# Optimization experiments

Hardware: AMD Instinct MI355X
Metric: run time of the kernel (lower is better)

## Reference

```python
import jax, jax.numpy as jnp
import numpy as np

B, S, D = 4, 2048, 1024


def setup_inputs() -> dict:
    key = jax.random.key(0)
    ks = jax.random.split(key, 9)
    scale = 1.0 / np.sqrt(D)
    x = jax.random.normal(ks[0], (B, S, D), dtype=jnp.float32)
    # causal mask (batch, seq, seq), int32; positions with 0 are masked out
    mask = jnp.broadcast_to(jnp.tril(jnp.ones((S, S), dtype=jnp.int32)), (B, S, S))
    Wq = jax.random.uniform(ks[1], (D, D), jnp.float32, -scale, scale)
    bq = jax.random.uniform(ks[2], (D,), jnp.float32, -scale, scale)
    Wk = jax.random.uniform(ks[3], (D, D), jnp.float32, -scale, scale)
    bk = jax.random.uniform(ks[4], (D,), jnp.float32, -scale, scale)
    Wv = jax.random.uniform(ks[5], (D, D), jnp.float32, -scale, scale)
    bv = jax.random.uniform(ks[6], (D,), jnp.float32, -scale, scale)
    Wo = jax.random.uniform(ks[7], (D, D), jnp.float32, -scale, scale)
    bo = jax.random.uniform(ks[8], (D,), jnp.float32, -scale, scale)
    return {"x": x, "mask": mask, "Wq": Wq, "bq": bq, "Wk": Wk, "bk": bk,
            "Wv": Wv, "bv": bv, "Wo": Wo, "bo": bo}


def reference(x, mask, Wq, bq, Wk, bk, Wv, bv, Wo, bo):
    d_model = x.shape[-1]
    scaling = jnp.sqrt(jnp.asarray(d_model, dtype=jnp.float32))
    # torch nn.Linear: y = x @ W.T + b
    Q = jnp.einsum('bsd,ed->bse', x, Wq) + bq
    K = jnp.einsum('bsd,ed->bse', x, Wk) + bk
    V = jnp.einsum('bsd,ed->bse', x, Wv) + bv
    scores = jnp.einsum('bqd,bkd->bqk', Q, K) / scaling  # (B, S, S)
    scores = jnp.where(mask == 0, jnp.float32(-1e9), scores)
    attn = jax.nn.softmax(scores, axis=2)
    out = jnp.einsum('bqk,bkd->bqd', attn, V)
    out = jnp.einsum('bsd,ed->bse', out, Wo) + bo
    return out, attn
```

## Files before the change

### kernel.cpp

```cpp
#include <hip/hip_runtime.h>
#include <hip/hip_bf16.h>
#include <stdint.h>


typedef unsigned short u16;
typedef __attribute__((ext_vector_type(8))) __bf16 bf16x8;
typedef __attribute__((ext_vector_type(4))) float f32x4;

__device__ __forceinline__ u16 f2bf(float f) {
  unsigned int u = __builtin_bit_cast(unsigned int, f);
  u = u + 0x7FFFu + ((u >> 16) & 1u);
  return (u16)(u >> 16);
}

__device__ __forceinline__ float bf2f(u16 u) {
  unsigned int w = ((unsigned int)u) << 16;
  return __builtin_bit_cast(float, w);
}

__device__ __forceinline__ void gl_lds16(const void* g, void* l) {
  __builtin_amdgcn_global_load_lds(
      (const __attribute__((address_space(1))) void*)g,
      (__attribute__((address_space(3))) void*)l, 16, 0, 0);
}

#define MFMA(a, b, c) __builtin_amdgcn_mfma_f32_16x16x32_bf16((a), (b), (c), 0, 0, 0)

#define TILE 128
#define BKK  64
template<int GM, int GX, int OUTMODE, bool BIAS, bool CKB, int NTT>
__global__ __launch_bounds__(256) void gemm_bt(
    const u16* __restrict__ A, const u16* __restrict__ Bmat,
    const float* __restrict__ b0, const float* __restrict__ b1,
    const float* __restrict__ b2,
    void* __restrict__ C0, u16* __restrict__ C1, u16* __restrict__ C2,
    int N, int K, long long sAb, long long sBb, long long sCb, int nchunk) {
  __shared__ __align__(16) u16 As[2][TILE * BKK];
  __shared__ __align__(16) u16 Bs[2][TILE * BKK];
  const int bid = blockIdx.x;
  int bx, by, bz;
  if (GM == 1) {
    const int lidx = (bid & 7) * nchunk + (bid >> 3);
    bz = lidx / 136;
    const int i = lidx - bz * 136;
    by = (int)((sqrtf(8.f * i + 1.f) - 1.f) * 0.5f);
    while ((by + 1) * (by + 2) / 2 <= i) ++by;
    while (by * (by + 1) / 2 > i) --by;
    bx = i - by * (by + 1) / 2;
  } else if (GM == 3) {
    const int j = bid & 255;
    const int k = j >> 5;
    by = (bid >> 8) ? k : 15 - k;
    bz = (j & 31) >> 3;
    bx = j & 7;
  } else if (GM == 4) {
    const int xcd = bid & 7, c = bid >> 3;
    bz = 0;
    by = xcd * 8 + (c >> 3);
    bx = c & 7;
  } else {
    const int lidx = (bid & 7) * 64 + (bid >> 3);
    bz = lidx >> 7;
    by = (lidx & 127) >> 4;
    bx = lidx & 15;
  }
  const int t = threadIdx.x;
  const int lane = t & 63, wid = t >> 6;
  const int wm = (wid >> 1) * 64, wn = (wid & 1) * 64;
  const int fr = lane & 15, fh = lane >> 4;

  const char* Ab = (const char*)(A + (size_t)bz * sAb + (size_t)by * TILE * K);
  const size_t rowstride = (size_t)K * 2;
  const size_t BOFF = (size_t)8 * TILE * rowstride;
  const char* Btile = (const char*)(Bmat + (size_t)bz * sBb + (size_t)bx * TILE * K);

  int srow[4], scol[4], slin[4];
#pragma unroll
  for (int c = 0; c < 4; ++c) {
    slin[c] = c * 4096 + t * 16;
    srow[c] = slin[c] >> 7;
    scol[c] = (slin[c] & 127) ^ ((srow[c] & 7) << 4);
  }

  int Keff = K;
  if (CKB) { int kb2 = (by + 1) * TILE; Keff = kb2 < K ? kb2 : K; }
  const int nkt = Keff / BKK;

#define STAGE(ko_, buf_, Bp_)                                                 \
  {                                                                           \
    _Pragma("unroll") for (int c = 0; c < 4; ++c) {                           \
      gl_lds16(Ab + (size_t)srow[c] * rowstride + (ko_) + scol[c],            \
               (char*)As[buf_] + slin[c]);                                    \
      gl_lds16((Bp_) + (size_t)srow[c] * rowstride + (ko_) + scol[c],         \
               (char*)Bs[buf_] + slin[c]);                                    \
    }                                                                         \
  }

  STAGE(0, 0, Btile)
  __syncthreads();

  int cur = 0;
  for (int tt = 0; tt < NTT; ++tt) {
    f32x4 acc[4][4];
#pragma unroll
    for (int m = 0; m < 4; ++m)
#pragma unroll
      for (int n = 0; n < 4; ++n) acc[m][n] = {0.f, 0.f, 0.f, 0.f};

    for (int kt = 0; kt < nkt; ++kt) {
      const bool last = (kt + 1 == nkt);
      if (!last) {
        STAGE((size_t)(kt + 1) * (BKK * 2), cur ^ 1, Btile)
      } else if (NTT > 1 && tt + 1 < NTT) {
        STAGE(0, cur ^ 1, Btile + BOFF)
      }
      const char* Ac = (const char*)As[cur];
      const char* Bc = (const char*)Bs[cur];
#pragma unroll
      for (int kk = 0; kk < BKK; kk += 32) {
        bf16x8 af[4], bg[4];
#pragma unroll
        for (int m = 0; m < 4; ++m) {
          int r = wm + m * 16 + fr;
          int cb = (kk * 2 + fh * 16) ^ ((r & 7) << 4);
          af[m] = *(const bf16x8*)(Ac + r * 128 + cb);
        }
#pragma unroll
        for (int n = 0; n < 4; ++n) {
          int r = wn + n * 16 + fr;
          int cb = (kk * 2 + fh * 16) ^ ((r & 7) << 4);
          bg[n] = *(const bf16x8*)(Bc + r * 128 + cb);
        }
#pragma unroll
        for (int m = 0; m < 4; ++m)
#pragma unroll
          for (int n = 0; n < 4; ++n)
            acc[m][n] = MFMA(af[m], bg[n], acc[m][n]);
      }
      if (!last) __syncthreads();
      cur ^= 1;
    }

    const int bxe = bx + 8 * tt;
    const int gm0 = by * TILE + wm, gn0 = bxe * TILE + wn;
#pragma unroll
    for (int n = 0; n < 4; ++n) {
      const int gc = gn0 + n * 16 + fr;
      float bvv = 0.f;
      if (BIAS) {
        if (OUTMODE == 3) {
          const int w = bxe >> 3;
          bvv = (w == 0 ? b0 : w == 1 ? b1 : b2)[gc & 1023];
        } else {
          bvv = b0[gc];
        }
      }
#pragma unroll
      for (int m = 0; m < 4; ++m) {
        const int gr0 = gm0 + m * 16 + fh * 4;
        float v[4];
#pragma unroll
        for (int j = 0; j < 4; ++j) v[j] = acc[m][n][j] + bvv;
        if (OUTMODE == 1) {
          float* C = (float*)C0 + (size_t)bz * sCb;
#pragma unroll
          for (int j = 0; j < 4; ++j) C[(size_t)(gr0 + j) * N + gc] = v[j];
        } else if (OUTMODE == 0) {
          u16* C = (u16*)C0 + (size_t)bz * sCb;
#pragma unroll
          for (int j = 0; j < 4; ++j) C[(size_t)(gr0 + j) * N + gc] = f2bf(v[j]);
        } else {
          const int w = bxe >> 3;
          const int gcl = gc & 1023;
          u16* dst = (w == 0) ? (u16*)C0 : (w == 1) ? C1 : C2;
          const float sc = (w == 0) ? 0.03125f : 1.0f;
#pragma unroll
          for (int j = 0; j < 4; ++j)
            dst[(size_t)(gr0 + j) * 1024 + gcl] = f2bf(v[j] * sc);
        }
      }
    }

    if (NTT > 1 && tt + 1 < NTT) {
      __syncthreads();
      Btile += BOFF;
    }
  }
#undef STAGE
}

#define WGFENCE asm volatile("" ::: "memory")
#define WGBAR()                         \
  {                                     \
    WGFENCE;                            \
    __builtin_amdgcn_s_barrier();       \
    WGFENCE;                            \
  }
#define LGKM0                                              \
  {                                                        \
    asm volatile("s_waitcnt lgkmcnt(0)" ::: "memory");     \
    __builtin_amdgcn_sched_barrier(0);                     \
  }
#define VMC(n_) asm volatile("s_waitcnt vmcnt(" #n_ ")" ::: "memory")

#define STG(dst_, srcb_, kt_, kh_)                                            \
  {                                                                           \
    _Pragma("unroll") for (int c_ = 0; c_ < 2; ++c_)                          \
        gl_lds16((srcb_) + (size_t)(c_ * 128 + srow0) * 2048 +                \
                     (kt_) * 128 + (kh_) * 64 + scol16,                       \
                 (char*)(dst_) + c_ * 8192 + t * 16);                         \
  }
#define LDA(slot_, mh_)                                                       \
  {                                                                           \
    _Pragma("unroll") for (int m_ = 0; m_ < 4; ++m_) {                        \
      const int r_ = WR + (mh_) * 64 + m_ * 16 + fr;                          \
      af[m_] = *(const bf16x8*)((const char*)(slot_) + r_ * 64 + fb);         \
    }                                                                         \
  }
#define LDB(slot_)                                                            \
  {                                                                           \
    _Pragma("unroll") for (int n_ = 0; n_ < 4; ++n_) {                        \
      const int r_ = WC + n_ * 16 + fr;                                       \
      bg[n_] = *(const bf16x8*)((const char*)(slot_) + r_ * 64 + fb);         \
    }                                                                         \
  }
#define MMAP(mh_)                                                             \
  {                                                                           \
    _Pragma("unroll") for (int m_ = 0; m_ < 4; ++m_)                          \
        _Pragma("unroll") for (int n_ = 0; n_ < 4; ++n_)                      \
            acc[(mh_) * 4 + m_][n_] =                                         \
                MFMA(af[m_], bg[n_], acc[(mh_) * 4 + m_][n_]);                \
  }
#define PHASE(CUR, KH, MH, DOB, VMSTMT, ...)   \
  {                                            \
    if (DOB) LDB(Bs[CUR][KH]);                 \
    LDA(As[CUR][KH], MH);                      \
    __VA_ARGS__;                               \
    WGBAR();                                   \
    LGKM0;                                     \
    __builtin_amdgcn_s_setprio(1);             \
    MMAP(MH);                                  \
    __builtin_amdgcn_s_setprio(0);             \
    VMSTMT;                                    \
    WGBAR();                                   \
  }

template <int LAUNCH>
__global__ __launch_bounds__(512, 2) void gemm256(
    const u16* __restrict__ xb, const u16* __restrict__ wqkb,
    const u16* __restrict__ wvb, const u16* __restrict__ wob,
    u16* __restrict__ qb, u16* __restrict__ kb, u16* __restrict__ vr,
    u16* __restrict__ pb, u16* __restrict__ vtb,
    const float* __restrict__ bq, const float* __restrict__ bk,
    const float* __restrict__ bv) {
  __shared__ __align__(16) u16 As[2][2][8192];
  __shared__ __align__(16) u16 Bs[2][2][8192];

  const int bid = blockIdx.x;
  const u16* Au;
  const u16* Bu;
  u16* Cu;
  const float* bias = nullptr;
  float scale = 1.f;
  int ldc, crow, ccol;
  if (LAUNCH == 0) {
    const int lidx = (bid & 7) * 32 + (bid >> 3);
    const int by = lidx >> 3, bx = lidx & 7;
    Au = xb + (size_t)by * 256 * 1024;
    Bu = wqkb + (size_t)bx * 256 * 1024;
    const int w = bx >> 2;
    Cu = w ? kb : qb;
    ldc = 1024;
    crow = by * 256;
    ccol = (bx & 3) * 256;
    bias = w ? bk : bq;
    scale = w ? 1.f : 0.03125f;
  } else if (LAUNCH == 1) {
    if (bid < 128) {
      const int by = bid >> 2, bx = bid & 3;
      Au = xb + (size_t)by * 256 * 1024;
      Bu = wvb + (size_t)bx * 256 * 1024;
      Cu = vr;
      ldc = 1024;
      crow = by * 256;
      ccol = bx * 256;
      bias = bv;
    } else {
      const int s2 = bid - 128;
      const int bz = s2 / 28;
      const int i = s2 - bz * 28;
      int by = 1, a2 = 0;
      while (a2 + by <= i) { a2 += by; ++by; }
      const int bx = i - a2;
      Au = qb + ((size_t)bz * 2048 + by * 256) * 1024;
      Bu = kb + ((size_t)bz * 2048 + bx * 256) * 1024;
      Cu = pb + (size_t)bz * 2048 * 2048;
      ldc = 2048;
      crow = by * 256;
      ccol = bx * 256;
    }
  } else {
    if (bid < 32) {
      const int bz = bid >> 3, d = bid & 7;
      Au = qb + ((size_t)bz * 2048 + d * 256) * 1024;
      Bu = kb + ((size_t)bz * 2048 + d * 256) * 1024;
      Cu = pb + (size_t)bz * 2048 * 2048;
      ldc = 2048;
      crow = d * 256;
      ccol = d * 256;
    } else {
      const int s2 = bid - 32;
      const int bz = s2 >> 5, j = s2 & 31;
      const int dby = j >> 3, sbx = j & 7;
      Au = wob + (size_t)dby * 256 * 1024;
      Bu = vr + ((size_t)bz * 2048 + sbx * 256) * 1024;
      Cu = vtb + (size_t)bz * 1024 * 2048;
      ldc = 2048;
      crow = dby * 256;
      ccol = sbx * 256;
    }
  }

  const int t = threadIdx.x;
  const int lane = t & 63, wid = t >> 6;
  const int WR = (wid >> 2) * 128, WC = (wid & 3) * 64;
  const int fr = lane & 15, fh = lane >> 4;
  const int fb = (fh ^ ((fr >> 1) & 3)) << 4;
  const int srow0 = t >> 2;
  const int scol16 = ((t & 3) ^ ((t >> 3) & 3)) << 4;
  const char* Abase = (const char*)Au;
  const char* Bbase = (const char*)Bu;

  f32x4 acc[8][4];
#pragma unroll
  for (int mi = 0; mi < 8; ++mi)
#pragma unroll
    for (int n = 0; n < 4; ++n) acc[mi][n] = {0.f, 0.f, 0.f, 0.f};
  bf16x8 af[4], bg[4];

  STG(As[0][0], Abase, 0, 0)
  STG(Bs[0][0], Bbase, 0, 0)
  STG(Bs[0][1], Bbase, 0, 1)
  STG(As[0][1], Abase, 0, 1)
  STG(Bs[1][0], Bbase, 1, 0)
  STG(As[1][0], Abase, 1, 0)
  STG(Bs[1][1], Bbase, 1, 1)
  VMC(10);
  WGBAR();

  for (int kt = 0; kt < 14; ++kt) {
    const int cur = kt & 1;
    PHASE(cur, 0, 0, true, (void)0, STG(As[cur ^ 1][1], Abase, kt + 1, 1))
    PHASE(cur, 0, 1, false, VMC(10), STG(Bs[cur][0], Bbase, kt + 2, 0))
    PHASE(cur, 1, 0, true, (void)0, STG(As[cur][0], Abase, kt + 2, 0))
    PHASE(cur, 1, 1, false, VMC(10), STG(Bs[cur][1], Bbase, kt + 2, 1))
  }
  PHASE(0, 0, 0, true, (void)0, STG(As[1][1], Abase, 15, 1))
  PHASE(0, 0, 1, false, VMC(8), (void)0)
  PHASE(0, 1, 0, true, (void)0, (void)0)
  PHASE(0, 1, 1, false, VMC(4), (void)0)
  PHASE(1, 0, 0, true, (void)0, (void)0)
  PHASE(1, 0, 1, false, VMC(0), (void)0)
  PHASE(1, 1, 0, true, (void)0, (void)0)
  PHASE(1, 1, 1, false, (void)0, (void)0)

  const int gr0 = crow + WR, gc0 = ccol + WC;
#pragma unroll
  for (int n = 0; n < 4; ++n) {
    const int gc = gc0 + n * 16 + fr;
    const float bb = bias ? bias[gc] : 0.f;
#pragma unroll
    for (int mi = 0; mi < 8; ++mi) {
      const int grr = gr0 + mi * 16 + fh * 4;
#pragma unroll
      for (int j = 0; j < 4; ++j)
        Cu[(size_t)(grr + j) * ldc + gc] = f2bf((acc[mi][n][j] + bb) * scale);
    }
  }
}

__global__ __launch_bounds__(256) void cvt_all(
    const float4* __restrict__ x, ushort4* __restrict__ xb,
    const float4* __restrict__ w0, const float4* __restrict__ w1,
    const float4* __restrict__ w2, const float4* __restrict__ w3,
    ushort4* __restrict__ o0, ushort4* __restrict__ o1,
    ushort4* __restrict__ o2, ushort4* __restrict__ o3) {
  int i = blockIdx.x * 256 + threadIdx.x;
  const float4* src;
  ushort4* dst;
  int idx;
  if (i < 2097152) {
    src = x; dst = xb; idx = i;
  } else {
    int j = i - 2097152;
    int w = j >> 18;
    idx = j & 262143;
    src = (w == 0) ? w0 : (w == 1) ? w1 : (w == 2) ? w2 : w3;
    dst = (w == 0) ? o0 : (w == 1) ? o1 : (w == 2) ? o2 : o3;
  }
  float4 v = src[idx];
  ushort4 o;
  o.x = f2bf(v.x); o.y = f2bf(v.y); o.z = f2bf(v.z); o.w = f2bf(v.w);
  dst[idx] = o;
}

__global__ __launch_bounds__(256) void softmax_rows(
    u16* __restrict__ pb, float* __restrict__ attnF) {
  const int row = blockIdx.x;
  const int q = row & 2047;
  const int nv = q + 1;
  const int nvt = (q & ~127) + 128;
  const int t = threadIdx.x;
  u16* brow = pb + (size_t)row * 2048;
  float* srow = attnF + (size_t)row * 2048;
  __shared__ float red[4];

  const int e0 = 8 * t;
  float a[8];
  if (e0 < nvt) {
    ushort4 u0 = ((const ushort4*)brow)[2 * t];
    ushort4 u1 = ((const ushort4*)brow)[2 * t + 1];
    u16 us[8] = {u0.x, u0.y, u0.z, u0.w, u1.x, u1.y, u1.z, u1.w};
#pragma unroll
    for (int j = 0; j < 8; ++j)
      a[j] = (e0 + j < nv) ? bf2f(us[j]) : -3.0e38f;
  } else {
#pragma unroll
    for (int j = 0; j < 8; ++j) a[j] = -3.0e38f;
  }

  float lmax = -3.0e38f;
#pragma unroll
  for (int j = 0; j < 8; ++j) lmax = fmaxf(lmax, a[j]);
#pragma unroll
  for (int o = 32; o > 0; o >>= 1) lmax = fmaxf(lmax, __shfl_xor(lmax, o));
  if ((t & 63) == 0) red[t >> 6] = lmax;
  __syncthreads();
  const float m = fmaxf(fmaxf(red[0], red[1]), fmaxf(red[2], red[3]));
  __syncthreads();

  float lsum = 0.f;
#pragma unroll
  for (int j = 0; j < 8; ++j) {
    a[j] = __expf(a[j] - m);
    lsum += a[j];
  }
#pragma unroll
  for (int o = 32; o > 0; o >>= 1) lsum += __shfl_xor(lsum, o);
  if ((t & 63) == 0) red[t >> 6] = lsum;
  __syncthreads();
  const float inv = 1.f / (red[0] + red[1] + red[2] + red[3]);

#pragma unroll
  for (int j = 0; j < 8; ++j) a[j] *= inv;
  ((float4*)srow)[2 * t]     = float4{a[0], a[1], a[2], a[3]};
  ((float4*)srow)[2 * t + 1] = float4{a[4], a[5], a[6], a[7]};
  if (e0 < nvt) {
    ushort4 ba; ba.x = f2bf(a[0]); ba.y = f2bf(a[1]); ba.z = f2bf(a[2]); ba.w = f2bf(a[3]);
    ushort4 bb; bb.x = f2bf(a[4]); bb.y = f2bf(a[5]); bb.z = f2bf(a[6]); bb.w = f2bf(a[7]);
    ((ushort4*)brow)[2 * t]     = ba;
    ((ushort4*)brow)[2 * t + 1] = bb;
  }
}

extern "C" void kernel_launch(void* const* d_in, const int* in_sizes, int n_in,
                              void* d_out, int out_size, void* d_ws,
                              size_t ws_size, hipStream_t stream) {
  (void)in_sizes; (void)n_in; (void)out_size; (void)ws_size;
  const int B = 4, S = 2048, D = 1024;
  const float* x  = (const float*)d_in[0];
  const float* Wq = (const float*)d_in[2]; const float* bq = (const float*)d_in[3];
  const float* Wk = (const float*)d_in[4]; const float* bk = (const float*)d_in[5];
  const float* Wv = (const float*)d_in[6]; const float* bv = (const float*)d_in[7];
  const float* Wo = (const float*)d_in[8]; const float* bo = (const float*)d_in[9];

  float* out  = (float*)d_out;
  float* attn = out + (size_t)B * S * D;

  char* ws = (char*)d_ws;
  u16* xb  = (u16*)(ws);
  u16* wqb = (u16*)(ws + 16777216);
  u16* wkb = wqb + 1048576;
  u16* wvb = wkb + 1048576;
  u16* wob = wvb + 1048576;
  u16* qb  = (u16*)(ws + 25165824);
  u16* kb  = (u16*)(ws + 41943040);
  u16* vr  = (u16*)(ws + 58720256);
  u16* pb  = (u16*)(ws + 75497472);

  cvt_all<<<12288, 256, 0, stream>>>(
      (const float4*)x, (ushort4*)xb,
      (const float4*)Wq, (const float4*)Wk, (const float4*)Wv, (const float4*)Wo,
      (ushort4*)wqb, (ushort4*)wkb, (ushort4*)wvb, (ushort4*)wob);

  gemm256<0><<<256, 512, 0, stream>>>(xb, wqb, wvb, wob, qb, kb, vr, pb, xb,
                                      bq, bk, bv);

  gemm256<1><<<240, 512, 0, stream>>>(xb, wqb, wvb, wob, qb, kb, vr, pb, xb,
                                      bq, bk, bv);

  gemm256<2><<<160, 512, 0, stream>>>(xb, wqb, wvb, wob, qb, kb, vr, pb, xb,
                                      bq, bk, bv);

  softmax_rows<<<B * S, 256, 0, stream>>>(pb, attn);

  gemm_bt<3, 8, 1, true, true, 1><<<512, 256, 0, stream>>>(
      pb, xb, bo, nullptr, nullptr, out, nullptr, nullptr,
      1024, 2048, (long long)S * S, (long long)D * S, (long long)S * D, 0);
}
```

Measured before the change: 210.8 us.

## Double-buffer LDS fragment registers to overlap ds_reads with MFMA in GEMM

Restructures the 256x256 GEMM main loop so A/B fragments are read from LDS into alternating register banks (afA/afB, bgA/bgB) one phase ahead of their use. Partial lgkmcnt waits replace the full LDS drain, and one barrier per phase is removed, so LDS reads can overlap the previous phase's MFMAs. This costs extra VGPRs for the second fragment bank, which may pressure occupancy at 2 waves per SIMD, and the hand-counted waitcnt and buffer-reuse ordering becomes more fragile.

```diff
diff --git a/kernel.cpp b/kernel.cpp
--- a/kernel.cpp
+++ b/kernel.cpp
@@ -189,17 +189,11 @@
 #undef STAGE
 }
 
-#define WGFENCE asm volatile("" ::: "memory")
-#define WGBAR()                         \
-  {                                     \
-    WGFENCE;                            \
-    __builtin_amdgcn_s_barrier();       \
-    WGFENCE;                            \
-  }
-#define LGKM0                                              \
-  {                                                        \
-    asm volatile("s_waitcnt lgkmcnt(0)" ::: "memory");     \
-    __builtin_amdgcn_sched_barrier(0);                     \
+#define WGBAR()                                        \
+  {                                                    \
+    asm volatile("" ::: "memory");                     \
+    __builtin_amdgcn_s_barrier();                      \
+    asm volatile("" ::: "memory");                     \
   }
 #define VMC(n_) asm volatile("s_waitcnt vmcnt(" #n_ ")" ::: "memory")
 
@@ -210,39 +204,30 @@
                      (kt_) * 128 + (kh_) * 64 + scol16,                       \
                  (char*)(dst_) + c_ * 8192 + t * 16);                         \
   }
-#define LDA(slot_, mh_)                                                       \
+#define LDAm(bank_, slot_, mh_)                                               \
   {                                                                           \
     _Pragma("unroll") for (int m_ = 0; m_ < 4; ++m_) {                        \
       const int r_ = WR + (mh_) * 64 + m_ * 16 + fr;                          \
-      af[m_] = *(const bf16x8*)((const char*)(slot_) + r_ * 64 + fb);         \
+      bank_[m_] = *(const bf16x8*)((const char*)(slot_) + r_ * 64 + fb);      \
     }                                                                         \
   }
-#define LDB(slot_)                                                            \
+#define LDBm(bank_, slot_)                                                    \
   {                                                                           \
     _Pragma("unroll") for (int n_ = 0; n_ < 4; ++n_) {                        \
       const int r_ = WC + n_ * 16 + fr;                                       \
-      bg[n_] = *(const bf16x8*)((const char*)(slot_) + r_ * 64 + fb);         \
+      bank_[n_] = *(const bf16x8*)((const char*)(slot_) + r_ * 64 + fb);      \
     }                                                                         \
   }
-#define MMAP(mh_)                                                             \
+#define PHT(LG_, AFB_, BGB_, MH_)                                             \
   {                                                                           \
+    asm volatile("s_waitcnt lgkmcnt(" #LG_ ")" ::: "memory");                 \
+    __builtin_amdgcn_sched_barrier(0);                                        \
+    __builtin_amdgcn_s_setprio(1);                                            \
     _Pragma("unroll") for (int m_ = 0; m_ < 4; ++m_)                          \
         _Pragma("unroll") for (int n_ = 0; n_ < 4; ++n_)                      \
-            acc[(mh_) * 4 + m_][n_] =                                         \
-                MFMA(af[m_], bg[n_], acc[(mh_) * 4 + m_][n_]);                \
-  }
-#define PHASE(CUR, KH, MH, DOB, VMSTMT, ...)   \
-  {                                            \
-    if (DOB) LDB(Bs[CUR][KH]);                 \
-    LDA(As[CUR][KH], MH);                      \
-    __VA_ARGS__;                               \
-    WGBAR();                                   \
-    LGKM0;                                     \
-    __builtin_amdgcn_s_setprio(1);             \
-    MMAP(MH);                                  \
-    __builtin_amdgcn_s_setprio(0);             \
-    VMSTMT;                                    \
-    WGBAR();                                   \
+            acc[(MH_) * 4 + m_][n_] =                                         \
+                MFMA(AFB_[m_], BGB_[n_], acc[(MH_) * 4 + m_][n_]);            \
+    __builtin_amdgcn_s_setprio(0);                                            \
   }
 
 template <int LAUNCH>
@@ -336,7 +321,7 @@
   for (int mi = 0; mi < 8; ++mi)
 #pragma unroll
     for (int n = 0; n < 4; ++n) acc[mi][n] = {0.f, 0.f, 0.f, 0.f};
-  bf16x8 af[4], bg[4];
+  bf16x8 afA[4], afB[4], bgA[4], bgB[4];
 
   STG(As[0][0], Abase, 0, 0)
   STG(Bs[0][0], Bbase, 0, 0)
@@ -347,22 +332,42 @@
   STG(Bs[1][1], Bbase, 1, 1)
   VMC(10);
   WGBAR();
-
-  for (int kt = 0; kt < 14; ++kt) {
-    const int cur = kt & 1;
-    PHASE(cur, 0, 0, true, (void)0, STG(As[cur ^ 1][1], Abase, kt + 1, 1))
-    PHASE(cur, 0, 1, false, VMC(10), STG(Bs[cur][0], Bbase, kt + 2, 0))
-    PHASE(cur, 1, 0, true, (void)0, STG(As[cur][0], Abase, kt + 2, 0))
-    PHASE(cur, 1, 1, false, VMC(10), STG(Bs[cur][1], Bbase, kt + 2, 1))
-  }
-  PHASE(0, 0, 0, true, (void)0, STG(As[1][1], Abase, 15, 1))
-  PHASE(0, 0, 1, false, VMC(8), (void)0)
-  PHASE(0, 1, 0, true, (void)0, (void)0)
-  PHASE(0, 1, 1, false, VMC(4), (void)0)
-  PHASE(1, 0, 0, true, (void)0, (void)0)
-  PHASE(1, 0, 1, false, VMC(0), (void)0)
-  PHASE(1, 1, 0, true, (void)0, (void)0)
-  PHASE(1, 1, 1, false, (void)0, (void)0)
+  LDBm(bgA, Bs[0][0])
+  LDAm(afA, As[0][0], 0)
+
+  for (int kt = 0; kt < 14; kt += 2) {
+    STG(As[1][1], Abase, kt + 1, 1) LDAm(afB, As[0][0], 1)
+    PHT(4, afA, bgA, 0) VMC(8); WGBAR();
+    STG(Bs[0][0], Bbase, kt + 2, 0) LDBm(bgB, Bs[0][1]) LDAm(afA, As[0][1], 0)
+    PHT(8, afB, bgA, 1) WGBAR();
+    STG(As[0][0], Abase, kt + 2, 0) LDAm(afB, As[0][1], 1)
+    PHT(4, afA, bgB, 0) VMC(8); WGBAR();
+    STG(Bs[0][1], Bbase, kt + 2, 1) LDBm(bgA, Bs[1][0]) LDAm(afA, As[1][0], 0)
+    PHT(8, afB, bgB, 1) WGBAR();
+    STG(As[0][1], Abase, kt + 2, 1) LDAm(afB, As[1][0], 1)
+    PHT(4, afA, bgA, 0) VMC(8); WGBAR();
+    STG(Bs[1][0], Bbase, kt + 3, 0) LDBm(bgB, Bs[1][1]) LDAm(afA, As[1][1], 0)
+    PHT(8, afB, bgA, 1) WGBAR();
+    STG(As[1][0], Abase, kt + 3, 0) LDAm(afB, As[1][1], 1)
+    PHT(4, afA, bgB, 0) VMC(8); WGBAR();
+    STG(Bs[1][1], Bbase, kt + 3, 1) LDBm(bgA, Bs[0][0]) LDAm(afA, As[0][0], 0)
+    PHT(8, afB, bgB, 1) WGBAR();
+  }
+  STG(As[1][1], Abase, 15, 1) LDAm(afB, As[0][0], 1)
+  PHT(4, afA, bgA, 0) VMC(8); WGBAR();
+  LDBm(bgB, Bs[0][1]) LDAm(afA, As[0][1], 0)
+  PHT(8, afB, bgA, 1) WGBAR();
+  LDAm(afB, As[0][1], 1)
+  PHT(4, afA, bgB, 0) VMC(4); WGBAR();
+  LDBm(bgA, Bs[1][0]) LDAm(afA, As[1][0], 0)
+  PHT(8, afB, bgB, 1) WGBAR();
+  LDAm(afB, As[1][0], 1)
+  PHT(4, afA, bgA, 0) VMC(0); WGBAR();
+  LDBm(bgB, Bs[1][1]) LDAm(afA, As[1][1], 0)
+  PHT(8, afB, bgA, 1) WGBAR();
+  LDAm(afB, As[1][1], 1)
+  PHT(4, afA, bgB, 0) WGBAR();
+  PHT(0, afB, bgB, 1) WGBAR();
 
   const int gr0 = crow + WR, gc0 = ccol + WC;
 #pragma unroll
```

Result: faster. 191.1 us (-9.4%).
